# Optimization experiments

Hardware: AMD Instinct MI355X
Metric: run time of the kernel (lower is better)

Reference implementation:

```python
import jax, jax.numpy as jnp
import numpy as np

PI = float(np.pi)


def _lsa_cols(cost):
    """Jonker-Volgenant / Hungarian on a square cost matrix (numpy float64).
    Returns col_ind such that (arange(n), col_ind) is the optimal assignment,
    matching scipy.optimize.linear_sum_assignment for a square matrix."""
    n = cost.shape[0]
    C = np.zeros((n + 1, n + 1), dtype=np.float64)
    C[1:, 1:] = cost
    u = np.zeros(n + 1)
    v = np.zeros(n + 1)
    p = np.zeros(n + 1, dtype=np.int64)  # p[j] = row matched to column j (1-indexed)
    for i in range(1, n + 1):
        p[0] = i
        j0 = 0
        minv = np.full(n + 1, np.inf)
        way = np.zeros(n + 1, dtype=np.int64)
        used = np.zeros(n + 1, dtype=bool)
        while True:
            used[j0] = True
            i0 = p[j0]
            cur = C[i0] - u[i0] - v
            upd = (~used) & (cur < minv)
            minv = np.where(upd, cur, minv)
            way[upd] = j0
            masked = np.where(used, np.inf, minv)
            j1 = int(np.argmin(masked))
            delta = masked[j1]
            u[p[used]] += delta
            v[used] -= delta
            minv[~used] -= delta
            j0 = j1
            if p[j0] == 0:
                break
        while j0:
            j1 = way[j0]
            p[j0] = p[j1]
            j0 = j1
    col_to_row = p[1:] - 1  # row assigned to each column
    col_ind = np.empty(n, dtype=np.int64)
    col_ind[col_to_row] = np.arange(n)
    return col_ind


def _batched_assignment(input, target):
    # cdist p=2 : (B, N, N)
    diff = input[:, :, None, :] - target[:, None, :, :]
    cost = jnp.sqrt(jnp.sum(diff * diff, axis=-1))
    cost_np = np.asarray(cost, dtype=np.float64)
    # serial per-sample Hungarian solve (mirrors the original scipy loop)
    cols = np.stack([_lsa_cols(cost_np[b]) for b in range(cost_np.shape[0])], axis=0)
    return jnp.asarray(cols)  # (B, N)


def setup_inputs() -> dict:
    key = jax.random.key(0)
    k1, k2 = jax.random.split(key)
    B, N, D = 128, 128, 5
    return {
        "input": jax.random.normal(k1, (B, N, D), dtype=jnp.float32),
        "target": jax.random.normal(k2, (B, N, D), dtype=jnp.float32),
    }


def reference(input, target):
    cols = _batched_assignment(input, target)  # (B, N), constant w.r.t. grads
    # row_ind is identity (square matrix), so aligned_pred == input;
    # aligned_true = target gathered by the optimal columns.
    aligned_true = jnp.take_along_axis(target, cols[:, :, None], axis=1)
    d = input - aligned_true
    x_loss = jnp.mean(d[..., 0] ** 2)
    y_loss = jnp.mean(d[..., 1] ** 2)
    E_loss = jnp.mean(d[..., 2] ** 2)
    theta_loss = jnp.mean(d[..., 3] ** 2)
    phi_diff = jnp.remainder(d[..., 4] + PI, 2.0 * PI) - PI  # wrap to (-pi, pi]
    phi_loss = jnp.mean(phi_diff ** 2)
    total_loss = x_loss + y_loss + E_loss + theta_loss + phi_loss
    # [total, x, y, E, theta, phi]
    return jnp.stack([total_loss, x_loss, y_loss, E_loss, theta_loss, phi_loss])
```

## Files before the change

### kernel.cpp

```cpp
#include <hip/hip_runtime.h>

#define NN 128
#define NB 128
#define ND 5
#define INFV 3.4028235e38f

__device__ __forceinline__ float wrap_phi(float x) {
  const float PI_F   = 3.14159265358979323846f;
  const float TWO_PI = 6.28318530717958647692f;
  float t = x + PI_F;
  float w = t - floorf(t * (1.0f / TWO_PI)) * TWO_PI;
  return w - PI_F;
}

#define DPP_SRC_INF(x, ctrl, rmask)                                           \
  __int_as_float(__builtin_amdgcn_update_dpp(                                 \
      0x7f800000, __float_as_int(x), (ctrl), (rmask), 0xF, false))

#define DPP_MIN_STEP(x, ctrl, rmask) x = fminf(x, DPP_SRC_INF(x, ctrl, rmask))

#define DPP_MIN2_STEP(x1, x2, ctrl, rmask)                                    \
  { float _a1 = DPP_SRC_INF(x1, ctrl, rmask);                                 \
    float _a2 = DPP_SRC_INF(x2, ctrl, rmask);                                 \
    float _t  = fmaxf(x1, _a1);                                               \
    x1 = fminf(x1, _a1);                                                      \
    x2 = fminf(fminf(x2, _a2), _t); }

__device__ __forceinline__ int rl_i(int v, int lane) {
  return __builtin_amdgcn_readlane(v, lane);
}
__device__ __forceinline__ float rl_f(float v, int lane) {
  return __int_as_float(__builtin_amdgcn_readlane(__float_as_int(v), lane));
}

__device__ __forceinline__ float wave_min_bcast(float x) {
  DPP_MIN_STEP(x, 0xB1,  0xF);
  DPP_MIN_STEP(x, 0x4E,  0xF);
  DPP_MIN_STEP(x, 0x141, 0xF);
  DPP_MIN_STEP(x, 0x140, 0xF);
  DPP_MIN_STEP(x, 0x142, 0xA);
  DPP_MIN_STEP(x, 0x143, 0xC);
  return rl_f(x, 63);
}

__device__ __forceinline__ void wave_min2_bcast(float &x1, float &x2) {
  DPP_MIN2_STEP(x1, x2, 0xB1,  0xF);
  DPP_MIN2_STEP(x1, x2, 0x4E,  0xF);
  DPP_MIN2_STEP(x1, x2, 0x141, 0xF);
  DPP_MIN2_STEP(x1, x2, 0x140, 0xF);
  DPP_MIN2_STEP(x1, x2, 0x142, 0xA);
  DPP_MIN2_STEP(x1, x2, 0x143, 0xC);
  x1 = rl_f(x1, 63);
  x2 = rl_f(x2, 63);
}

__global__ __launch_bounds__(64) void set2set_hungarian(
    const float* __restrict__ inp, const float* __restrict__ tgt,
    float* __restrict__ sums)
{
  const int b = blockIdx.x;
  const int lane = threadIdx.x;

  __shared__ __align__(16) float Csh[NN * NN];
  __shared__ float inpS[NN * ND];
  __shared__ int   rowOwner[NN + 1];
  __shared__ float uFree[NN + 1];

  const float* inB = inp + (size_t)b * NN * ND;
  const float* tgB = tgt + (size_t)b * NN * ND;

  for (int idx = lane; idx < NN * ND; idx += 64) inpS[idx] = inB[idx];
  for (int idx = lane; idx <= NN; idx += 64) { rowOwner[idx] = 0x7fffffff; uFree[idx] = 0.f; }
  __syncthreads();

  const int jA = 2 * lane;
  const int jB = 2 * lane + 1;
  const int c1A = jA + 1, c1B = jB + 1;

  float tA[ND], tB[ND];
  #pragma unroll
  for (int d = 0; d < ND; ++d) { tA[d] = tgB[jA * ND + d]; tB[d] = tgB[jB * ND + d]; }

  float vA = INFV, vB = INFV;
  int   rmA = 1,  rmB = 1;
  #pragma unroll 4
  for (int i = 0; i < NN; ++i) {
    float sA = 0.f, sB = 0.f;
    #pragma unroll
    for (int d = 0; d < ND; ++d) {
      float x = inpS[i * ND + d];
      float da = x - tA[d]; sA = fmaf(da, da, sA);
      float db = x - tB[d]; sB = fmaf(db, db, sB);
    }
    float cA = sqrtf(sA), cB = sqrtf(sB);
    ((float2*)(Csh + i * NN))[lane] = make_float2(cA, cB);
    if (cA < vA) { vA = cA; rmA = i + 1; }
    if (cB < vB) { vB = cB; rmB = i + 1; }
  }
  __syncthreads();

  atomicMin(&rowOwner[rmA], c1A);
  atomicMin(&rowOwner[rmB], c1B);
  __syncthreads();

  int   pA = (rowOwner[rmA] == c1A) ? rmA : 0;
  int   pB = (rowOwner[rmB] == c1B) ? rmB : 0;
  float uA = 0.f, uB = 0.f;
  int   wayA = 0, wayB = 0;

  {
    unsigned long long mtA = __ballot(pA != 0);
    unsigned long long mtB = __ballot(pB != 0);
    while (mtA | mtB) {
      int l, slot;
      if (mtA) { l = __ffsll(mtA) - 1; mtA &= mtA - 1ull; slot = 0; }
      else     { l = __ffsll(mtB) - 1; mtB &= mtB - 1ull; slot = 1; }
      int owner = l;
      int i = rl_i(slot ? pB : pA, owner);
      const float2 c = ((const float2*)(Csh + (i - 1) * NN))[lane];
      float rA_ = c.x - vA, rB_ = c.y - vB;
      if (lane == owner) { if (slot) rB_ = INFV; else rA_ = INFV; }
      float mu = wave_min_bcast(fminf(rA_, rB_));
      bool selA = (lane == owner) && (slot == 0);
      bool selB = (lane == owner) && (slot == 1);
      vA -= selA ? mu : 0.f;   vB -= selB ? mu : 0.f;
      uA  = selA ? mu : uA;    uB  = selB ? mu : uB;
    }
  }

  unsigned long long remLo = __ballot(rowOwner[1 + lane]  == 0x7fffffff);
  unsigned long long remHi = __ballot(rowOwner[65 + lane] == 0x7fffffff);

  #pragma unroll 1
  for (int pass = 0; pass < 3; ++pass) {
    unsigned long long inLo = remLo, inHi = remHi;
    unsigned long long outLo = 0ull, outHi = 0ull;
    while (inLo | inHi) {
      int i;
      if (inLo) { int t = __ffsll(inLo) - 1; inLo &= inLo - 1ull; i = t + 1; }
      else      { int t = __ffsll(inHi) - 1; inHi &= inHi - 1ull; i = t + 65; }

      const float2 c = ((const float2*)(Csh + (i - 1) * NN))[lane];
      float rcA = c.x - vA, rcB = c.y - vB;
      float m1 = fminf(rcA, rcB), m2 = fmaxf(rcA, rcB);
      float candv = m1;
      bool  aMin  = (rcA <= rcB);
      int   candc = aMin ? c1A : c1B;
      int   candp = aMin ? pA : pB;
      float candu = aMin ? uA : uB;
      wave_min2_bcast(m1, m2);

      unsigned long long msk = __ballot(candv == m1);
      int l = __ffsll(msk) - 1;
      int   j1   = rl_i(candc, l);
      int   i0   = rl_i(candp, l);
      float uOld = rl_f(candu, l);
      int owner = l, slot = (j1 - 1) & 1;

      float dv = m2 - m1;
      bool selA = (lane == owner) && (slot == 0);
      bool selB = (lane == owner) && (slot == 1);
      vA -= selA ? dv : 0.f;   vB -= selB ? dv : 0.f;
      pA  = selA ? i  : pA;    pB  = selB ? i  : pB;
      uA  = selA ? m2 : uA;    uB  = selB ? m2 : uB;

      if (i0 != 0) {
        if (lane == 0) uFree[i0] = uOld;
        if (i0 <= 64) outLo |= 1ull << (i0 - 1);
        else          outHi |= 1ull << (i0 - 65);
      }
    }
    remLo = outLo; remHi = outHi;
  }
  unsigned long long dijLo = remLo, dijHi = remHi;

  while (dijLo | dijHi) {
    int i;
    if (dijLo) { int t = __ffsll(dijLo) - 1; dijLo &= dijLo - 1ull; i = t + 1; }
    else       { int t = __ffsll(dijHi) - 1; dijHi &= dijHi - 1ull; i = t + 65; }
    float uf = uFree[i];

    float dAllA = INFV, dAllB = INFV;
    float dLiveA = INFV, dLiveB = INFV;
    bool usedA = false, usedB = false;
    int   j0 = 0, i0 = i;
    float minVal = 0.f;
    float tshift = 0.f - uf;
    float tvA = tshift - vA, tvB = tshift - vB;
    int   jfree = 0;

    for (int guard = 0; guard <= NN + 1; ++guard) {
      const float2 c = ((const float2*)(Csh + (i0 - 1) * NN))[lane];
      float curA = c.x + tvA;
      float curB = c.y + tvB;
      bool okA = !usedA && (curA < dAllA);
      bool okB = !usedB && (curB < dAllB);
      dAllA  = okA ? curA : dAllA;   dLiveA = okA ? curA : dLiveA;
      wayA   = okA ? j0 : wayA;
      dAllB  = okB ? curB : dAllB;   dLiveB = okB ? curB : dLiveB;
      wayB   = okB ? j0 : wayB;

      float candv = fminf(dLiveA, dLiveB);
      bool  aMin  = (dLiveA <= dLiveB);
      int   candc = aMin ? c1A : c1B;
      int   candp = aMin ? pA : pB;
      float candu = aMin ? uA : uB;

      minVal = wave_min_bcast(candv);
      unsigned long long msk = __ballot(candv == minVal);
      int l = __ffsll(msk) - 1;
      int   j1  = rl_i(candc, l);
      int   pj1 = rl_i(candp, l);
      float uj  = rl_f(candu, l);
      if (pj1 == 0) { jfree = j1; break; }

      bool nowA = (j1 == c1A), nowB = (j1 == c1B);
      usedA |= nowA;  usedB |= nowB;
      dLiveA = nowA ? INFV : dLiveA;
      dLiveB = nowB ? INFV : dLiveB;
      tshift = minVal - uj;
      tvA = tshift - vA;  tvB = tshift - vB;
      j0 = j1; i0 = pj1;
    }

    {
      float adjA = dAllA - minVal;
      float adjB = dAllB - minVal;
      vA += usedA ? adjA : 0.f;   uA -= usedA ? adjA : 0.f;
      vB += usedB ? adjB : 0.f;   uB -= usedB ? adjB : 0.f;
    }
    float ucur = uf + minVal;

    int jj = jfree;
    for (int g = 0; g < NN + 1 && jj != 0; ++g) {
      int owner = (jj - 1) >> 1, slot = (jj - 1) & 1;
      int wj = slot ? rl_i(wayB, owner) : rl_i(wayA, owner);
      int pnew; float unew;
      if (wj == 0) { pnew = i; unew = ucur; }
      else {
        int o2 = (wj - 1) >> 1, s2 = (wj - 1) & 1;
        pnew = s2 ? rl_i(pB, o2) : rl_i(pA, o2);
        unew = s2 ? rl_f(uB, o2) : rl_f(uA, o2);
      }
      bool selA = (lane == owner) && (slot == 0);
      bool selB = (lane == owner) && (slot == 1);
      pA = selA ? pnew : pA;  uA = selA ? unew : uA;
      pB = selB ? pnew : pB;  uB = selB ? unew : uB;
      jj = wj;
    }
  }

  int rA = pA - 1;
  int rB = pB - 1;
  float acc[ND];
  #pragma unroll
  for (int d = 0; d < ND; ++d) {
    float dA = inpS[rA * ND + d] - tA[d];
    float dB = inpS[rB * ND + d] - tB[d];
    if (d == 4) { dA = wrap_phi(dA); dB = wrap_phi(dB); }
    acc[d] = dA * dA + dB * dB;
  }
  #pragma unroll
  for (int d = 0; d < ND; ++d) {
    float s = acc[d];
    #pragma unroll
    for (int off = 32; off > 0; off >>= 1) s += __shfl_xor(s, off);
    if (lane == 0) atomicAdd(&sums[d], s);
  }
}

__global__ void set2set_finalize(const float* __restrict__ sums, float* __restrict__ out) {
  const float inv = 1.0f / (128.0f * 128.0f);
  float x  = sums[0] * inv;
  float y  = sums[1] * inv;
  float E  = sums[2] * inv;
  float th = sums[3] * inv;
  float ph = sums[4] * inv;
  out[1] = x; out[2] = y; out[3] = E; out[4] = th; out[5] = ph;
  out[0] = x + y + E + th + ph;
}

extern "C" void kernel_launch(void* const* d_in, const int* in_sizes, int n_in,
                              void* d_out, int out_size, void* d_ws, size_t ws_size,
                              hipStream_t stream) {
  const float* inp = (const float*)d_in[0];
  const float* tgt = (const float*)d_in[1];
  float* out  = (float*)d_out;
  float* sums = (float*)d_ws;

  hipMemsetAsync(sums, 0, ND * sizeof(float), stream);
  set2set_hungarian<<<dim3(NB), dim3(64), 0, stream>>>(inp, tgt, sums);
  set2set_finalize<<<dim3(1), dim3(1), 0, stream>>>(sums, out);
}
```

Before: 391.1 us.

## Use multi-source Dijkstra augmentation seeded from all free rows

Each augmentation phase now starts the shortest-path search from every remaining free row at once, seeding the column distances with their reduced costs minus each row's dual. The free row that the found path reaches is tracked per column (src) and is removed from the free set after augmentation. The aim is fewer and shorter Dijkstra searches, since the nearest free column is found across all free rows together. In exchange, every phase pays a seeding pass over all remaining free rows, and per-phase work and path lengths may vary.

```diff
diff --git a/kernel.cpp b/kernel.cpp
--- a/kernel.cpp
+++ b/kernel.cpp
@@ -107,6 +107,7 @@
   int   pB = (rowOwner[rmB] == c1B) ? rmB : 0;
   float uA = 0.f, uB = 0.f;
   int   wayA = 0, wayB = 0;
+  int   srcA = 0, srcB = 0;
 
   {
     unsigned long long mtA = __ballot(pA != 0);
@@ -175,31 +176,45 @@
   unsigned long long dijLo = remLo, dijHi = remHi;
 
   while (dijLo | dijHi) {
-    int i;
-    if (dijLo) { int t = __ffsll(dijLo) - 1; dijLo &= dijLo - 1ull; i = t + 1; }
-    else       { int t = __ffsll(dijHi) - 1; dijHi &= dijHi - 1ull; i = t + 65; }
-    float uf = uFree[i];
-
     float dAllA = INFV, dAllB = INFV;
-    float dLiveA = INFV, dLiveB = INFV;
+    float dLiveA, dLiveB;
     bool usedA = false, usedB = false;
-    int   j0 = 0, i0 = i;
+    wayA = 0; wayB = 0; srcA = 0; srcB = 0;
+
+    {
+      unsigned long long mLo = dijLo, mHi = dijHi;
+      while (mLo | mHi) {
+        int ia, ib = 0;
+        if (mLo) { int t = __ffsll(mLo) - 1; mLo &= mLo - 1ull; ia = t + 1; }
+        else     { int t = __ffsll(mHi) - 1; mHi &= mHi - 1ull; ia = t + 65; }
+        if (mLo)      { int t = __ffsll(mLo) - 1; mLo &= mLo - 1ull; ib = t + 1; }
+        else if (mHi) { int t = __ffsll(mHi) - 1; mHi &= mHi - 1ull; ib = t + 65; }
+
+        float nufa = 0.f - uFree[ia];
+        const float2 ca = ((const float2*)(Csh + (ia - 1) * NN))[lane];
+        float nufb = 0.f;
+        float2 cb = make_float2(0.f, 0.f);
+        if (ib) {
+          nufb = 0.f - uFree[ib];
+          cb = ((const float2*)(Csh + (ib - 1) * NN))[lane];
+        }
+        float cAa = (ca.x - vA) + nufa, cBa = (ca.y - vB) + nufa;
+        bool okA = cAa < dAllA, okB = cBa < dAllB;
+        dAllA = okA ? cAa : dAllA;  srcA = okA ? ia : srcA;
+        dAllB = okB ? cBa : dAllB;  srcB = okB ? ia : srcB;
+        if (ib) {
+          float cAb = (cb.x - vA) + nufb, cBb = (cb.y - vB) + nufb;
+          bool okA2 = cAb < dAllA, okB2 = cBb < dAllB;
+          dAllA = okA2 ? cAb : dAllA;  srcA = okA2 ? ib : srcA;
+          dAllB = okB2 ? cBb : dAllB;  srcB = okB2 ? ib : srcB;
+        }
+      }
+      dLiveA = dAllA; dLiveB = dAllB;
+    }
+
     float minVal = 0.f;
-    float tshift = 0.f - uf;
-    float tvA = tshift - vA, tvB = tshift - vB;
     int   jfree = 0;
-
     for (int guard = 0; guard <= NN + 1; ++guard) {
-      const float2 c = ((const float2*)(Csh + (i0 - 1) * NN))[lane];
-      float curA = c.x + tvA;
-      float curB = c.y + tvB;
-      bool okA = !usedA && (curA < dAllA);
-      bool okB = !usedB && (curB < dAllB);
-      dAllA  = okA ? curA : dAllA;   dLiveA = okA ? curA : dLiveA;
-      wayA   = okA ? j0 : wayA;
-      dAllB  = okB ? curB : dAllB;   dLiveB = okB ? curB : dLiveB;
-      wayB   = okB ? j0 : wayB;
-
       float candv = fminf(dLiveA, dLiveB);
       bool  aMin  = (dLiveA <= dLiveB);
       int   candc = aMin ? c1A : c1B;
@@ -218,9 +233,18 @@
       usedA |= nowA;  usedB |= nowB;
       dLiveA = nowA ? INFV : dLiveA;
       dLiveB = nowB ? INFV : dLiveB;
-      tshift = minVal - uj;
-      tvA = tshift - vA;  tvB = tshift - vB;
-      j0 = j1; i0 = pj1;
+      float tshift = minVal - uj;
+      float tvA = tshift - vA, tvB = tshift - vB;
+
+      const float2 c = ((const float2*)(Csh + (pj1 - 1) * NN))[lane];
+      float curA = c.x + tvA;
+      float curB = c.y + tvB;
+      bool okA = !usedA && (curA < dAllA);
+      bool okB = !usedB && (curB < dAllB);
+      dAllA  = okA ? curA : dAllA;  dLiveA = okA ? curA : dLiveA;
+      wayA   = okA ? j1 : wayA;
+      dAllB  = okB ? curB : dAllB;  dLiveB = okB ? curB : dLiveB;
+      wayB   = okB ? j1 : wayB;
     }
 
     {
@@ -229,15 +253,19 @@
       vA += usedA ? adjA : 0.f;   uA -= usedA ? adjA : 0.f;
       vB += usedB ? adjB : 0.f;   uB -= usedB ? adjB : 0.f;
     }
-    float ucur = uf + minVal;
 
     int jj = jfree;
+    int matchedSrc = 0;
     for (int g = 0; g < NN + 1 && jj != 0; ++g) {
       int owner = (jj - 1) >> 1, slot = (jj - 1) & 1;
       int wj = slot ? rl_i(wayB, owner) : rl_i(wayA, owner);
       int pnew; float unew;
-      if (wj == 0) { pnew = i; unew = ucur; }
-      else {
+      if (wj == 0) {
+        int isrc = slot ? rl_i(srcB, owner) : rl_i(srcA, owner);
+        pnew = isrc;
+        unew = uFree[isrc] + minVal;
+        matchedSrc = isrc;
+      } else {
         int o2 = (wj - 1) >> 1, s2 = (wj - 1) & 1;
         pnew = s2 ? rl_i(pB, o2) : rl_i(pA, o2);
         unew = s2 ? rl_f(uB, o2) : rl_f(uA, o2);
@@ -248,6 +276,11 @@
       pB = selB ? pnew : pB;  uB = selB ? unew : uB;
       jj = wj;
     }
+
+    if (matchedSrc) {
+      if (matchedSrc <= 64) dijLo &= ~(1ull << (matchedSrc - 1));
+      else                  dijHi &= ~(1ull << (matchedSrc - 65));
+    }
   }
 
   int rA = pA - 1;
```

New measurement: 430.8 us. +10.1%, slower.

## Unroll reduction-transfer loop by two with frozen column duals; double augmentation-row passes

Applied to the files above, without the earlier changes.

Processes two matched rows per iteration of the reduction-transfer step and computes reduced costs against a snapshot of the column duals taken before the loop, so two independent wave-min reductions and shared-memory loads can overlap. Using stale duals changes the algorithm slightly, since row duals may be less tight. The auction/augmenting-row-reduction pass count is raised from three to six, which may settle more rows before the expensive augmentation but adds work if the passes don't converge.

```diff
diff --git a/kernel.cpp b/kernel.cpp
--- a/kernel.cpp
+++ b/kernel.cpp
@@ -109,22 +109,40 @@
   int   wayA = 0, wayB = 0;
 
   {
+    const float vOldA = vA, vOldB = vB;
     unsigned long long mtA = __ballot(pA != 0);
     unsigned long long mtB = __ballot(pB != 0);
     while (mtA | mtB) {
-      int l, slot;
-      if (mtA) { l = __ffsll(mtA) - 1; mtA &= mtA - 1ull; slot = 0; }
-      else     { l = __ffsll(mtB) - 1; mtB &= mtB - 1ull; slot = 1; }
-      int owner = l;
-      int i = rl_i(slot ? pB : pA, owner);
-      const float2 c = ((const float2*)(Csh + (i - 1) * NN))[lane];
-      float rA_ = c.x - vA, rB_ = c.y - vB;
-      if (lane == owner) { if (slot) rB_ = INFV; else rA_ = INFV; }
-      float mu = wave_min_bcast(fminf(rA_, rB_));
-      bool selA = (lane == owner) && (slot == 0);
-      bool selB = (lane == owner) && (slot == 1);
-      vA -= selA ? mu : 0.f;   vB -= selB ? mu : 0.f;
-      uA  = selA ? mu : uA;    uB  = selB ? mu : uB;
+      int l1, s1;
+      if (mtA) { l1 = __ffsll(mtA) - 1; mtA &= mtA - 1ull; s1 = 0; }
+      else     { l1 = __ffsll(mtB) - 1; mtB &= mtB - 1ull; s1 = 1; }
+      int i1 = rl_i(s1 ? pB : pA, l1);
+      int l2 = -1, s2 = 0, i2 = 0;
+      if (mtA)      { l2 = __ffsll(mtA) - 1; mtA &= mtA - 1ull; s2 = 0; }
+      else if (mtB) { l2 = __ffsll(mtB) - 1; mtB &= mtB - 1ull; s2 = 1; }
+      if (l2 >= 0) i2 = rl_i(s2 ? pB : pA, l2);
+
+      const float2 c1 = ((const float2*)(Csh + (i1 - 1) * NN))[lane];
+      float2 c2 = make_float2(0.f, 0.f);
+      if (i2) c2 = ((const float2*)(Csh + (i2 - 1) * NN))[lane];
+
+      float r1A = c1.x - vOldA, r1B = c1.y - vOldB;
+      if (lane == l1) { if (s1) r1B = INFV; else r1A = INFV; }
+      float mu1 = wave_min_bcast(fminf(r1A, r1B));
+      bool e1A = (lane == l1) && (s1 == 0);
+      bool e1B = (lane == l1) && (s1 == 1);
+      vA -= e1A ? mu1 : 0.f;   vB -= e1B ? mu1 : 0.f;
+      uA  = e1A ? mu1 : uA;    uB  = e1B ? mu1 : uB;
+
+      if (i2) {
+        float r2A = c2.x - vOldA, r2B = c2.y - vOldB;
+        if (lane == l2) { if (s2) r2B = INFV; else r2A = INFV; }
+        float mu2 = wave_min_bcast(fminf(r2A, r2B));
+        bool e2A = (lane == l2) && (s2 == 0);
+        bool e2B = (lane == l2) && (s2 == 1);
+        vA -= e2A ? mu2 : 0.f;   vB -= e2B ? mu2 : 0.f;
+        uA  = e2A ? mu2 : uA;    uB  = e2B ? mu2 : uB;
+      }
     }
   }
 
@@ -132,7 +150,7 @@
   unsigned long long remHi = __ballot(rowOwner[65 + lane] == 0x7fffffff);
 
   #pragma unroll 1
-  for (int pass = 0; pass < 3; ++pass) {
+  for (int pass = 0; pass < 6; ++pass) {
     unsigned long long inLo = remLo, inHi = remHi;
     unsigned long long outLo = 0ull, outHi = 0ull;
     while (inLo | inHi) {
```

Result: faster. 371.6 us, median of 2 (-5.0%).
